# Optimization experiments

Measured on AMD Instinct MI355X. Metric: run time of the kernel, lower is better.

## Reference

```python
import jax, jax.numpy as jnp
import numpy as np

B, S, D, H = 8, 1024, 768, 12
DH = D // H
EPS = 1e-5


def setup_inputs() -> dict:
    key = jax.random.key(0)
    ks = jax.random.split(key, 12)
    sc_h = 1.0 / np.sqrt(DH)
    sc_d = 1.0 / np.sqrt(D)
    return {
        "x": jax.random.normal(ks[0], (B, S, D), jnp.float32),
        "ln1_g": jnp.ones((D,), jnp.float32),
        "ln1_b": jnp.zeros((D,), jnp.float32),
        "Wq": jax.random.normal(ks[1], (H, DH, DH), jnp.float32) * sc_h,
        "bq": jax.random.normal(ks[2], (H, DH), jnp.float32) * 0.01,
        "Wk": jax.random.normal(ks[3], (H, DH, DH), jnp.float32) * sc_h,
        "bk": jax.random.normal(ks[4], (H, DH), jnp.float32) * 0.01,
        "Wv": jax.random.normal(ks[5], (H, DH, DH), jnp.float32) * sc_h,
        "bv": jax.random.normal(ks[6], (H, DH), jnp.float32) * 0.01,
        "ln2_g": jnp.ones((D,), jnp.float32),
        "ln2_b": jnp.zeros((D,), jnp.float32),
        "W1": jax.random.normal(ks[7], (D, 4 * D), jnp.float32) * sc_d,  # c_fc (bias=False)
        "W2": jax.random.normal(ks[8], (4 * D, D), jnp.float32) * (1.0 / np.sqrt(4 * D)),  # c_proj (bias=False)
    }


def _layernorm(x, g, b):
    m = jnp.mean(x, axis=-1, keepdims=True)
    v = jnp.mean(jnp.square(x - m), axis=-1, keepdims=True)
    return (x - m) * jax.lax.rsqrt(v + EPS) * g + b


def _msa(x, Wq, bq, Wk, bk, Wv, bv):
    b, s, d = x.shape
    h = x.reshape(b, s, H, DH)  # per-head slices of the embedding
    q = jnp.einsum('bshd,hde->bhse', h, Wq) + bq[None, :, None, :]
    k = jnp.einsum('bshd,hde->bhse', h, Wk) + bk[None, :, None, :]
    v = jnp.einsum('bshd,hde->bhse', h, Wv) + bv[None, :, None, :]
    scores = jnp.einsum('bhse,bhte->bhst', q, k) / np.sqrt(DH).astype(np.float32)
    attn = jax.nn.softmax(scores, axis=-1)
    o = jnp.einsum('bhst,bhte->bhse', attn, v)
    return o.transpose(0, 2, 1, 3).reshape(b, s, d)  # concat heads


def reference(x, ln1_g, ln1_b, Wq, bq, Wk, bk, Wv, bv, ln2_g, ln2_b, W1, W2):
    out = x + _msa(_layernorm(x, ln1_g, ln1_b), Wq, bq, Wk, bk, Wv, bv)
    h = _layernorm(out, ln2_g, ln2_b)
    ffn = jnp.dot(jax.nn.gelu(jnp.dot(h, W1), approximate=False), W2)
    return out + ffn
```

## Files before the change

kernel.cpp:

```cpp
#include <hip/hip_runtime.h>
#include <hip/hip_bf16.h>
#include <math.h>

#define B_ 8
#define S_ 1024
#define D_ 768
#define H_ 12
#define QSCALE 0.18033688011112042f

typedef __attribute__((ext_vector_type(8))) short short8;
typedef __attribute__((ext_vector_type(4))) float floatx4;
typedef unsigned short ushort_t;

__device__ __forceinline__ ushort_t f2bf(float f) {
  unsigned int u = __builtin_bit_cast(unsigned int, f);
  u += 0x7fffu + ((u >> 16) & 1u);
  return (ushort_t)(u >> 16);
}

__device__ __forceinline__ unsigned int pkbf(float a, float b) {
  __hip_bfloat162 h = __float22bfloat162_rn(make_float2(a, b));
  unsigned int r;
  __builtin_memcpy(&r, &h, sizeof(r));
  return r;
}

__device__ __forceinline__ float gelu_f(float x) {
  const float z = fabsf(x) * 0.70710678118654752f;
  const float t = __builtin_amdgcn_rcpf(1.0f + 0.3275911f * z);
  const float p =
      t * (0.254829592f +
           t * (-0.284496736f +
                t * (1.421413741f + t * (-1.453152027f + t * 1.061405429f))));
  const float e = __expf(-z * z);
  const float erfv = 1.0f - p * e;
  return 0.5f * x * (1.0f + copysignf(erfv, x));
}

template <int N>
__device__ __forceinline__ void wait_vmcnt() {
  if constexpr (N == 0)
    asm volatile("s_waitcnt vmcnt(0)" ::: "memory");
  else if constexpr (N == 3)
    asm volatile("s_waitcnt vmcnt(3)" ::: "memory");
  else if constexpr (N == 4)
    asm volatile("s_waitcnt vmcnt(4)" ::: "memory");
  else if constexpr (N == 6)
    asm volatile("s_waitcnt vmcnt(6)" ::: "memory");
  else
    asm volatile("s_waitcnt vmcnt(8)" ::: "memory");
}

__global__ __launch_bounds__(256) void ln_bf16(
    const float* __restrict__ in, const float* __restrict__ g,
    const float* __restrict__ bias, ushort_t* __restrict__ out) {
  const int row = blockIdx.x * 4 + (threadIdx.x >> 6);
  const int lane = threadIdx.x & 63;
  const float* p = in + (size_t)row * D_;
  float4 v[3];
#pragma unroll
  for (int j = 0; j < 3; ++j) v[j] = *(const float4*)(p + j * 256 + lane * 4);
  float s = 0.f;
#pragma unroll
  for (int j = 0; j < 3; ++j) s += (v[j].x + v[j].y) + (v[j].z + v[j].w);
#pragma unroll
  for (int m = 1; m < 64; m <<= 1) s += __shfl_xor(s, m);
  const float mean = s * (1.0f / D_);
  float q = 0.f;
#pragma unroll
  for (int j = 0; j < 3; ++j) {
    const float a = v[j].x - mean, b = v[j].y - mean;
    const float c = v[j].z - mean, d = v[j].w - mean;
    q += (a * a + b * b) + (c * c + d * d);
  }
#pragma unroll
  for (int m = 1; m < 64; m <<= 1) q += __shfl_xor(q, m);
  const float rstd = rsqrtf(q * (1.0f / D_) + 1e-5f);
  ushort_t* o = out + (size_t)row * D_;
#pragma unroll
  for (int j = 0; j < 3; ++j) {
    const float4 gv = *(const float4*)(g + j * 256 + lane * 4);
    const float4 bv = *(const float4*)(bias + j * 256 + lane * 4);
    const unsigned int p01 = pkbf((v[j].x - mean) * rstd * gv.x + bv.x,
                                  (v[j].y - mean) * rstd * gv.y + bv.y);
    const unsigned int p23 = pkbf((v[j].z - mean) * rstd * gv.z + bv.z,
                                  (v[j].w - mean) * rstd * gv.w + bv.w);
    *(uint2*)(o + j * 256 + lane * 4) = make_uint2(p01, p23);
  }
}

__device__ __forceinline__ void tcast_body(
    const float* __restrict__ W, ushort_t* __restrict__ Wt,
    int Kdim, int Ndim, int bx, int by, float* sh) {
  float(*tile)[33] = (float(*)[33])sh;
  const int n0 = bx * 32, k0 = by * 32;
  const int tx = threadIdx.x & 31, ty = threadIdx.x >> 5;
#pragma unroll
  for (int i = 0; i < 32; i += 8)
    tile[ty + i][tx] = W[(size_t)(k0 + ty + i) * Ndim + n0 + tx];
  __syncthreads();
#pragma unroll
  for (int i = 0; i < 32; i += 8)
    Wt[(size_t)(n0 + ty + i) * Kdim + k0 + tx] = f2bf(tile[tx][ty + i]);
}

__global__ __launch_bounds__(256) void prep_weights(
    const float* __restrict__ W1, ushort_t* __restrict__ Wt1,
    const float* __restrict__ W2, ushort_t* __restrict__ Wt2,
    const float* __restrict__ Wq, const float* __restrict__ Wk,
    const float* __restrict__ Wv, ushort_t* __restrict__ Wqt,
    ushort_t* __restrict__ Wkt, ushort_t* __restrict__ Wvt) {
  __shared__ float sh[64 * 65];
  const int bid = blockIdx.x;
  if (bid < 2304) {
    tcast_body(W1, Wt1, 768, 3072, bid % 96, bid / 96, sh);
  } else if (bid < 4608) {
    const int idx = bid - 2304;
    tcast_body(W2, Wt2, 3072, 768, idx % 24, idx / 24, sh);
  } else {
    const int idx = bid - 4608;
    const int h = idx % 12, which = idx / 12;
    const float* W = which == 0 ? Wq : which == 1 ? Wk : Wv;
    ushort_t* O = which == 0 ? Wqt : which == 1 ? Wkt : Wvt;
    float(*t)[65] = (float(*)[65])sh;
    const int tid = threadIdx.x;
#pragma unroll
    for (int i = 0; i < 16; ++i) {
      const int idx2 = tid + i * 256;
      t[idx2 >> 6][idx2 & 63] = W[h * 4096 + idx2];
    }
    __syncthreads();
#pragma unroll
    for (int i = 0; i < 16; ++i) {
      const int idx2 = tid + i * 256;
      O[h * 4096 + idx2] = f2bf(t[idx2 & 63][idx2 >> 6]);
    }
  }
}

__global__ __launch_bounds__(256) void qkv_mfma(
    const ushort_t* __restrict__ xbf,
    const ushort_t* __restrict__ Wqt, const ushort_t* __restrict__ Wkt,
    const ushort_t* __restrict__ Wvt,
    const float* __restrict__ bq, const float* __restrict__ bk,
    const float* __restrict__ bv,
    ushort_t* __restrict__ qo, ushort_t* __restrict__ ko,
    ushort_t* __restrict__ vt) {
  const int h = blockIdx.y;
  const int mb = blockIdx.x * 128;
  const int tid = threadIdx.x;
  const int wave = tid >> 6, lane = tid & 63;
  const int lc = lane & 15, kq = lane >> 4;
  const int wm = wave * 32;

  __shared__ __align__(16) ushort_t Lb[4][2560];
  ushort_t* Lw = Lb[wave];

  short8 af[2][2];
#pragma unroll
  for (int mi = 0; mi < 2; ++mi)
#pragma unroll
    for (int kc = 0; kc < 2; ++kc)
      af[mi][kc] = *(const short8*)(xbf + (size_t)(mb + wm + mi * 16 + lc) * D_ +
                                    h * 64 + kc * 32 + kq * 8);

  const ushort_t* Wp[3] = {Wqt + h * 4096, Wkt + h * 4096, Wvt + h * 4096};
  floatx4 accT[2][2][4] = {};
  floatx4 accV[2][4] = {};
#pragma unroll
  for (int n = 0; n < 4; ++n)
#pragma unroll
    for (int kc = 0; kc < 2; ++kc) {
      const short8 wq_ = *(const short8*)(Wp[0] + (n * 16 + lc) * 64 +
                                          kc * 32 + kq * 8);
      const short8 wk_ = *(const short8*)(Wp[1] + (n * 16 + lc) * 64 +
                                          kc * 32 + kq * 8);
      const short8 wv_ = *(const short8*)(Wp[2] + (n * 16 + lc) * 64 +
                                          kc * 32 + kq * 8);
#pragma unroll
      for (int mi = 0; mi < 2; ++mi) {
        accT[0][mi][n] = __builtin_amdgcn_mfma_f32_16x16x32_bf16(
            wq_, af[mi][kc], accT[0][mi][n], 0, 0, 0);
        accT[1][mi][n] = __builtin_amdgcn_mfma_f32_16x16x32_bf16(
            wk_, af[mi][kc], accT[1][mi][n], 0, 0, 0);
        accV[mi][n] = __builtin_amdgcn_mfma_f32_16x16x32_bf16(
            af[mi][kc], wv_, accV[mi][n], 0, 0, 0);
      }
    }

  const int b = mb >> 10;
  const size_t obase = (size_t)(b * H_ + h) * (S_ * 64);
  const int sbase = (mb & 1023) + wm;

#pragma unroll
  for (int w3 = 0; w3 < 2; ++w3) {
    const float* bias = (w3 == 0 ? bq : bk) + h * 64;
    ushort_t* outp = w3 == 0 ? qo : ko;
#pragma unroll
    for (int mi = 0; mi < 2; ++mi)
#pragma unroll
      for (int n = 0; n < 4; ++n) {
        const float4 bv4 = *(const float4*)(bias + n * 16 + kq * 4);
        const floatx4 v = accT[w3][mi][n];
        float v0 = v[0] + bv4.x, v1 = v[1] + bv4.y;
        float v2 = v[2] + bv4.z, v3 = v[3] + bv4.w;
        if (w3 == 0) { v0 *= QSCALE; v1 *= QSCALE; v2 *= QSCALE; v3 *= QSCALE; }
        *(uint2*)(&Lw[(mi * 16 + lc) * 72 + n * 16 + kq * 4]) =
            make_uint2(pkbf(v0, v1), pkbf(v2, v3));
      }
    asm volatile("s_waitcnt lgkmcnt(0)" ::: "memory");
    const int srow = lane >> 2, c16 = (lane & 3) * 16;
#pragma unroll
    for (int it = 0; it < 2; ++it) {
      const int s = it * 16 + srow;
      const uint4 r0 = *(const uint4*)(&Lw[s * 72 + c16]);
      const uint4 r1 = *(const uint4*)(&Lw[s * 72 + c16 + 8]);
      *(uint4*)(outp + obase + (size_t)(sbase + s) * 64 + c16) = r0;
      *(uint4*)(outp + obase + (size_t)(sbase + s) * 64 + c16 + 8) = r1;
    }
    asm volatile("s_waitcnt lgkmcnt(0)" ::: "memory");
  }

#pragma unroll
  for (int n = 0; n < 4; ++n) {
    const float bvv = bv[h * 64 + n * 16 + lc];
#pragma unroll
    for (int mi = 0; mi < 2; ++mi) {
      const floatx4 v = accV[mi][n];
      *(uint2*)(&Lw[(n * 16 + lc) * 40 + mi * 16 + kq * 4]) =
          make_uint2(pkbf(v[0] + bvv, v[1] + bvv),
                     pkbf(v[2] + bvv, v[3] + bvv));
    }
  }
  asm volatile("s_waitcnt lgkmcnt(0)" ::: "memory");
  {
    const int erow = lane >> 2, s8 = (lane & 3) * 8;
#pragma unroll
    for (int it = 0; it < 4; ++it) {
      const int e = it * 16 + erow;
      const uint4 r0 = *(const uint4*)(&Lw[e * 40 + s8]);
      *(uint4*)(vt + obase + (size_t)e * S_ + sbase + s8) = r0;
    }
  }
}

__global__ __launch_bounds__(512) void attn_mfma(
    const ushort_t* __restrict__ qb, const ushort_t* __restrict__ kb,
    const ushort_t* __restrict__ vt, const float* __restrict__ x,
    float* __restrict__ out1) {
  const int bh = blockIdx.x;
  const int tid = threadIdx.x;
  const int wave = tid >> 6, lane = tid & 63;
  const int lc = lane & 15, kq = lane >> 4;
  const int q0 = blockIdx.y * 128 + wave * 16;

  __shared__ __align__(16) ushort_t smem[8192 + 8 * 16 * 72];
  ushort_t* Ks = smem;
  ushort_t* Vs = smem + 4096;
  ushort_t* Pp = smem + 8192 + wave * (16 * 72);

  const ushort_t* qp = qb + (size_t)bh * (S_ * 64);
  const ushort_t* kp = kb + (size_t)bh * (S_ * 64);
  const ushort_t* vp = vt + (size_t)bh * (S_ * 64);

  short8 qf[2];
#pragma unroll
  for (int kc = 0; kc < 2; ++kc)
    qf[kc] = *(const short8*)(qp + (size_t)(q0 + lc) * 64 + kc * 32 + kq * 8);

  const int srow = tid >> 3;
  const int sgc = ((tid & 7) ^ (srow & 7)) * 8;
  const int slds = srow * 64 + (tid & 7) * 8;
  const int swz = lc & 7;

  float l_r = 0.0f;
  floatx4 oacc[4] = {};

  for (int kt = 0; kt < 16; ++kt) {
    __builtin_amdgcn_global_load_lds(
        (const __attribute__((address_space(1))) unsigned int*)
            (kp + (size_t)(kt * 64 + srow) * 64 + sgc),
        (__attribute__((address_space(3))) unsigned int*)(Ks + slds), 16, 0, 0);
    __builtin_amdgcn_global_load_lds(
        (const __attribute__((address_space(1))) unsigned int*)
            (vp + (size_t)srow * S_ + kt * 64 + sgc),
        (__attribute__((address_space(3))) unsigned int*)(Vs + slds), 16, 0, 0);
    __syncthreads();

    floatx4 sacc[4] = {};
#pragma unroll
    for (int mi = 0; mi < 4; ++mi) {
      const int row = (mi * 16 + lc) * 64;
#pragma unroll
      for (int kc = 0; kc < 2; ++kc) {
        const short8 kf =
            *(const short8*)(Ks + row + ((kc * 4 + kq) ^ swz) * 8);
        sacc[mi] = __builtin_amdgcn_mfma_f32_16x16x32_bf16(
            kf, qf[kc], sacc[mi], 0, 0, 0);
      }
    }

    float pr[4][4];
    float sm = 0.f;
#pragma unroll
    for (int mi = 0; mi < 4; ++mi)
#pragma unroll
      for (int r = 0; r < 4; ++r) {
        pr[mi][r] = exp2f(sacc[mi][r]);
        sm += pr[mi][r];
      }
    l_r += sm;
#pragma unroll
    for (int mi = 0; mi < 4; ++mi) {
      const unsigned int p01 = pkbf(pr[mi][0], pr[mi][1]);
      const unsigned int p23 = pkbf(pr[mi][2], pr[mi][3]);
      *(uint2*)(&Pp[lc * 72 + mi * 16 + kq * 4]) = make_uint2(p01, p23);
    }
    asm volatile("s_waitcnt lgkmcnt(0)" ::: "memory");

    short8 pf[2];
#pragma unroll
    for (int kc = 0; kc < 2; ++kc)
      pf[kc] = *(const short8*)(&Pp[lc * 72 + kc * 32 + kq * 8]);
#pragma unroll
    for (int mi = 0; mi < 4; ++mi) {
      const int row = (mi * 16 + lc) * 64;
#pragma unroll
      for (int kc = 0; kc < 2; ++kc) {
        const short8 vf =
            *(const short8*)(Vs + row + ((kc * 4 + kq) ^ swz) * 8);
        oacc[mi] = __builtin_amdgcn_mfma_f32_16x16x32_bf16(
            vf, pf[kc], oacc[mi], 0, 0, 0);
      }
    }
    __syncthreads();
  }

  const int b = bh / H_, h = bh % H_;
  float lt = l_r;
  lt += __shfl_xor(lt, 16);
  lt += __shfl_xor(lt, 32);
  const float inv = 1.0f / lt;
  float* Ow = (float*)smem + wave * 1088;
#pragma unroll
  for (int mi = 0; mi < 4; ++mi) {
    floatx4 ov = oacc[mi];
    ov[0] *= inv; ov[1] *= inv; ov[2] *= inv; ov[3] *= inv;
    *(floatx4*)(&Ow[lc * 68 + mi * 16 + kq * 4]) = ov;
  }
  asm volatile("s_waitcnt lgkmcnt(0)" ::: "memory");
  const int row = (lane >> 3) & 7, c8 = (lane & 7) * 4;
#pragma unroll
  for (int rg = 0; rg < 2; ++rg) {
    const int qq = rg * 8 + row;
    const size_t gbase =
        ((size_t)(b * S_) + q0 + qq) * D_ + h * 64 + c8;
#pragma unroll
    for (int j = 0; j < 2; ++j) {
      const float4 ov = *(const float4*)(&Ow[qq * 68 + j * 32 + c8]);
      const float4 xv = *(const float4*)(x + gbase + j * 32);
      *(float4*)(out1 + gbase + j * 32) =
          make_float4(ov.x + xv.x, ov.y + xv.y, ov.z + xv.z, ov.w + xv.w);
    }
  }
}

template <int BM, int BN, int N, int K, bool GELU, bool RESID, bool OUT_BF16>
__global__ __launch_bounds__(512, 2) void gemm_tbuf(
    const ushort_t* __restrict__ A, const ushort_t* __restrict__ Bt,
    const float* __restrict__ resid, void* __restrict__ Cout) {
  constexpr int LPTA = BM / 64;
  constexpr int LPTB = BN / 64;
  constexpr int LPT = LPTA + LPTB;
  constexpr int NT = K / 64;
  constexpr int TSZ = (BM + BN) * 64;

  const int nb = blockIdx.x * BN;
  const int mb = blockIdx.y * BM;
  const int tid = threadIdx.x;
  const int wave = tid >> 6, lane = tid & 63;
  const int wm = (wave >> 1) * 64;
  const int wn = (wave & 1) * 64;

  __shared__ __align__(16) ushort_t Ls[3][TSZ];

  const int sr = tid >> 3;
  const int sc8 = (tid & 7) * 8;
  const int sgx = ((tid & 7) ^ (sr & 7)) * 8;

  auto stageAll = [&](int t, int buf) {
    const int kb = t * 64;
#pragma unroll
    for (int j = 0; j < LPTA; ++j) {
      const int row = j * 64 + sr;
      __builtin_amdgcn_global_load_lds(
          (const __attribute__((address_space(1))) unsigned int*)
              (A + (size_t)(mb + row) * K + kb + sgx),
          (__attribute__((address_space(3))) unsigned int*)
              (&Ls[buf][row * 64 + sc8]), 16, 0, 0);
    }
#pragma unroll
    for (int j = 0; j < LPTB; ++j) {
      const int row = j * 64 + sr;
      __builtin_amdgcn_global_load_lds(
          (const __attribute__((address_space(1))) unsigned int*)
              (Bt + (size_t)(nb + row) * K + kb + sgx),
          (__attribute__((address_space(3))) unsigned int*)
              (&Ls[buf][BM * 64 + row * 64 + sc8]), 16, 0, 0);
    }
  };

  stageAll(0, 0);
  stageAll(1, 1);
  wait_vmcnt<LPT>();
  __builtin_amdgcn_s_barrier();
  __builtin_amdgcn_sched_barrier(0);

  const int lc = lane & 15, kq = lane >> 4, swz = lc & 7;
  floatx4 acc[4][4] = {};

  int buf = 0;
#pragma unroll 1
  for (int t = 0; t < NT; ++t) {
    const ushort_t* As = &Ls[buf][0];
    const ushort_t* Bs = &Ls[buf][BM * 64];
    int nbuf = buf + 2; if (nbuf >= 3) nbuf -= 3;

    short8 af[4][2], bfr[4][2];
#pragma unroll
    for (int ks = 0; ks < 2; ++ks) {
#pragma unroll
      for (int i = 0; i < 4; ++i)
        af[i][ks] = *(const short8*)(As + (wm + i * 16 + lc) * 64 +
                                     ((ks * 4 + kq) ^ swz) * 8);
#pragma unroll
      for (int j = 0; j < 4; ++j)
        bfr[j][ks] = *(const short8*)(Bs + (wn + j * 16 + lc) * 64 +
                                      ((ks * 4 + kq) ^ swz) * 8);
    }
    if (t + 2 < NT) stageAll(t + 2, nbuf);
    __builtin_amdgcn_s_setprio(1);
#pragma unroll
    for (int ks = 0; ks < 2; ++ks)
#pragma unroll
      for (int i = 0; i < 4; ++i)
#pragma unroll
        for (int j = 0; j < 4; ++j)
          acc[i][j] = __builtin_amdgcn_mfma_f32_16x16x32_bf16(
              af[i][ks], bfr[j][ks], acc[i][j], 0, 0, 0);
    __builtin_amdgcn_s_setprio(0);
    if (t + 1 < NT) {
      if (t + 2 < NT)
        wait_vmcnt<LPT>();
      else
        wait_vmcnt<0>();
      __builtin_amdgcn_s_barrier();
      __builtin_amdgcn_sched_barrier(0);
    }
    buf = (buf == 2) ? 0 : buf + 1;
  }

  const int lcol = lane & 15, lr4 = (lane >> 4) * 4;
#pragma unroll
  for (int i = 0; i < 4; ++i)
#pragma unroll
    for (int r = 0; r < 4; ++r) {
      const int m = mb + wm + i * 16 + lr4 + r;
#pragma unroll
      for (int j = 0; j < 4; ++j) {
        const int col = nb + wn + j * 16 + lcol;
        float vv = acc[i][j][r];
        if (GELU) vv = gelu_f(vv);
        if (RESID) vv += resid[(size_t)m * N + col];
        if (OUT_BF16)
          ((ushort_t*)Cout)[(size_t)m * N + col] = f2bf(vv);
        else
          ((float*)Cout)[(size_t)m * N + col] = vv;
      }
    }
}

template <int BM, int BN, int N, int K, bool GELU, bool RESID, bool OUT_BF16,
          bool XCDMAP>
__global__ __launch_bounds__(512, 4) void gemm_pipe(
    const ushort_t* __restrict__ A, const ushort_t* __restrict__ Bt,
    const float* __restrict__ resid, void* __restrict__ Cout) {
  constexpr int MI = BM / 32;
  constexpr int NJ = BN / 64;
  constexpr int LPT = BM / 64 + BN / 64;
  constexpr int NT = K / 64;

  int mb, nb;
  if constexpr (XCDMAP) {
    const int lin = blockIdx.x;
    const int xcd = lin & 7, slot = lin >> 3;
    const int mbg = slot / (N / 128), nbi = slot - mbg * (N / 128);
    mb = (xcd * 16 + mbg) * 64;
    nb = nbi * 128;
  } else {
    nb = blockIdx.x * BN;
    mb = blockIdx.y * BM;
  }

  const int tid = threadIdx.x;
  const int wave = tid >> 6, lane = tid & 63;
  const int wm = (wave >> 2) * (BM / 2), wn = (wave & 3) * (BN / 4);

  __shared__ __align__(16) ushort_t Asp[2][BM * 64];
  __shared__ __align__(16) ushort_t Bsp[2][BN * 64];

  const int sr = tid >> 3;
  const int sc8 = (tid & 7) * 8;
  const int sgx = ((tid & 7) ^ (sr & 7)) * 8;

  auto stage = [&](int t, int buf) {
    const int kb = t * 64;
#pragma unroll
    for (int j = 0; j < BM / 64; ++j) {
      const int row = j * 64 + sr;
      __builtin_amdgcn_global_load_lds(
          (const __attribute__((address_space(1))) unsigned int*)
              (A + (size_t)(mb + row) * K + kb + sgx),
          (__attribute__((address_space(3))) unsigned int*)
              (&Asp[buf][row * 64 + sc8]), 16, 0, 0);
    }
#pragma unroll
    for (int j = 0; j < BN / 64; ++j) {
      const int row = j * 64 + sr;
      __builtin_amdgcn_global_load_lds(
          (const __attribute__((address_space(1))) unsigned int*)
              (Bt + (size_t)(nb + row) * K + kb + sgx),
          (__attribute__((address_space(3))) unsigned int*)
              (&Bsp[buf][row * 64 + sc8]), 16, 0, 0);
    }
  };

  stage(0, 0);
  stage(1, 1);
  wait_vmcnt<LPT>();
  __builtin_amdgcn_s_barrier();
  __builtin_amdgcn_sched_barrier(0);

  const int lc = lane & 15, kq = lane >> 4, swz = lc & 7;
  floatx4 acc[MI][NJ] = {};

#pragma unroll 1
  for (int t = 0; t < NT; ++t) {
    const int cur = t & 1;
    short8 af[MI][2], bfr[NJ][2];
#pragma unroll
    for (int ks = 0; ks < 2; ++ks) {
#pragma unroll
      for (int i = 0; i < MI; ++i)
        af[i][ks] = *(const short8*)(&Asp[cur][(wm + i * 16 + lc) * 64 +
                                               ((ks * 4 + kq) ^ swz) * 8]);
#pragma unroll
      for (int j = 0; j < NJ; ++j)
        bfr[j][ks] = *(const short8*)(&Bsp[cur][(wn + j * 16 + lc) * 64 +
                                                ((ks * 4 + kq) ^ swz) * 8]);
    }
    __builtin_amdgcn_s_setprio(1);
#pragma unroll
    for (int i = 0; i < MI; ++i)
#pragma unroll
      for (int j = 0; j < NJ; ++j)
        acc[i][j] = __builtin_amdgcn_mfma_f32_16x16x32_bf16(
            af[i][0], bfr[j][0], acc[i][j], 0, 0, 0);
    __builtin_amdgcn_s_setprio(0);
    asm volatile("s_waitcnt lgkmcnt(0)" ::: "memory");
    __builtin_amdgcn_sched_barrier(0);
    __builtin_amdgcn_s_barrier();
    __builtin_amdgcn_sched_barrier(0);
    if (t + 2 < NT) stage(t + 2, cur);
    __builtin_amdgcn_sched_barrier(0);
    if (t + 2 < NT)
      wait_vmcnt<LPT>();
    else if (t + 1 < NT)
      wait_vmcnt<0>();
    if (t + 1 < NT) {
      __builtin_amdgcn_s_barrier();
      __builtin_amdgcn_sched_barrier(0);
    }
    __builtin_amdgcn_s_setprio(1);
#pragma unroll
    for (int i = 0; i < MI; ++i)
#pragma unroll
      for (int j = 0; j < NJ; ++j)
        acc[i][j] = __builtin_amdgcn_mfma_f32_16x16x32_bf16(
            af[i][1], bfr[j][1], acc[i][j], 0, 0, 0);
    __builtin_amdgcn_s_setprio(0);
  }

  const int lcol = lane & 15, lr4 = (lane >> 4) * 4;
#pragma unroll
  for (int i = 0; i < MI; ++i)
#pragma unroll
    for (int r = 0; r < 4; ++r) {
      const int m = mb + wm + i * 16 + lr4 + r;
#pragma unroll
      for (int j = 0; j < NJ; ++j) {
        const int col = nb + wn + j * 16 + lcol;
        float vv = acc[i][j][r];
        if (GELU) vv = gelu_f(vv);
        if (RESID) vv += resid[(size_t)m * N + col];
        if (OUT_BF16)
          ((ushort_t*)Cout)[(size_t)m * N + col] = f2bf(vv);
        else
          ((float*)Cout)[(size_t)m * N + col] = vv;
      }
    }
}

extern "C" void kernel_launch(void* const* d_in, const int* in_sizes, int n_in,
                              void* d_out, int out_size, void* d_ws, size_t ws_size,
                              hipStream_t stream) {
  (void)in_sizes; (void)n_in; (void)out_size; (void)ws_size;
  const float* x     = (const float*)d_in[0];
  const float* ln1_g = (const float*)d_in[1];
  const float* ln1_b = (const float*)d_in[2];
  const float* Wq    = (const float*)d_in[3];
  const float* bq    = (const float*)d_in[4];
  const float* Wk    = (const float*)d_in[5];
  const float* bk    = (const float*)d_in[6];
  const float* Wv    = (const float*)d_in[7];
  const float* bv    = (const float*)d_in[8];
  const float* ln2_g = (const float*)d_in[9];
  const float* ln2_b = (const float*)d_in[10];
  const float* W1    = (const float*)d_in[11];
  const float* W2    = (const float*)d_in[12];
  float* out = (float*)d_out;

  const size_t n = (size_t)B_ * S_ * D_;
  ushort_t* u = (ushort_t*)d_ws;
  ushort_t* xbf  = u;
  ushort_t* qb   = xbf + n;
  ushort_t* kb   = qb + n;
  ushort_t* vt   = kb + n;
  ushort_t* xbf2 = vt + n;
  ushort_t* act  = xbf2 + n;
  ushort_t* Wt1  = act + (size_t)8192 * 3072;
  ushort_t* Wt2  = Wt1 + (size_t)3072 * 768;
  ushort_t* Wqt  = Wt2 + (size_t)768 * 3072;
  ushort_t* Wkt  = Wqt + H_ * 4096;
  ushort_t* Wvt  = Wkt + H_ * 4096;
  float* out1 = (float*)(Wvt + H_ * 4096);

  prep_weights<<<dim3(4644), dim3(256), 0, stream>>>(
      W1, Wt1, W2, Wt2, Wq, Wk, Wv, Wqt, Wkt, Wvt);
  ln_bf16<<<dim3(2048), dim3(256), 0, stream>>>(x, ln1_g, ln1_b, xbf);
  qkv_mfma<<<dim3(64, 12), dim3(256), 0, stream>>>(xbf, Wqt, Wkt, Wvt,
                                                   bq, bk, bv, qb, kb, vt);
  attn_mfma<<<dim3(96, 8), dim3(512), 0, stream>>>(qb, kb, vt, x, out1);
  ln_bf16<<<dim3(2048), dim3(256), 0, stream>>>(out1, ln2_g, ln2_b, xbf2);
  gemm_tbuf<256, 128, 3072, 768, true, false, true>
      <<<dim3(24, 32), dim3(512), 0, stream>>>(xbf2, Wt1, nullptr, act);
  gemm_pipe<64, 128, 768, 3072, false, true, false, true>
      <<<dim3(768), dim3(512), 0, stream>>>(act, Wt2, out1, out);
}
```

Before: 298.8 us.

## Split FFN1 GEMM K-step into four phased LDS-read/MFMA stages with staggered prefetch

Replaces the triple-buffered FFN1 GEMM with a variant using a 128x256 tile (waves arranged 2x4) and splits each K-step into four quadrant phases. Each phase loads part of the fragments from LDS, issues part of the next tile's global-to-LDS prefetch (A, then B halves), and runs a quarter of the MFMAs, with barriers between phases. The intent is to interleave LDS reads, global loads and matrix math more finely so they overlap better. It adds several extra workgroup barriers and lgkmcnt waits per K-step, which could stall waves.

```diff
diff --git a/kernel.cpp b/kernel.cpp
--- a/kernel.cpp
+++ b/kernel.cpp
@@ -365,13 +365,11 @@
   }
 }
 
-template <int BM, int BN, int N, int K, bool GELU, bool RESID, bool OUT_BF16>
-__global__ __launch_bounds__(512, 2) void gemm_tbuf(
+template <int N, int K, bool GELU, bool OUT_BF16>
+__global__ __launch_bounds__(512, 2) void gemm_8ph(
     const ushort_t* __restrict__ A, const ushort_t* __restrict__ Bt,
-    const float* __restrict__ resid, void* __restrict__ Cout) {
-  constexpr int LPTA = BM / 64;
-  constexpr int LPTB = BN / 64;
-  constexpr int LPT = LPTA + LPTB;
+    void* __restrict__ Cout) {
+  constexpr int BM = 128, BN = 256;
   constexpr int NT = K / 64;
   constexpr int TSZ = (BM + BN) * 64;
 
@@ -379,8 +377,8 @@
   const int mb = blockIdx.y * BM;
   const int tid = threadIdx.x;
   const int wave = tid >> 6, lane = tid & 63;
-  const int wm = (wave >> 1) * 64;
-  const int wn = (wave & 1) * 64;
+  const int wm = (wave >> 2) * 64;
+  const int wn = (wave & 3) * 64;
 
   __shared__ __align__(16) ushort_t Ls[3][TSZ];
 
@@ -388,10 +386,10 @@
   const int sc8 = (tid & 7) * 8;
   const int sgx = ((tid & 7) ^ (sr & 7)) * 8;
 
-  auto stageAll = [&](int t, int buf) {
+  auto stageA = [&](int t, int buf) {
     const int kb = t * 64;
 #pragma unroll
-    for (int j = 0; j < LPTA; ++j) {
+    for (int j = 0; j < 2; ++j) {
       const int row = j * 64 + sr;
       __builtin_amdgcn_global_load_lds(
           (const __attribute__((address_space(1))) unsigned int*)
@@ -399,9 +397,12 @@
           (__attribute__((address_space(3))) unsigned int*)
               (&Ls[buf][row * 64 + sc8]), 16, 0, 0);
     }
-#pragma unroll
-    for (int j = 0; j < LPTB; ++j) {
-      const int row = j * 64 + sr;
+  };
+  auto stageB = [&](int t, int buf, int half) {
+    const int kb = t * 64;
+#pragma unroll
+    for (int j = 0; j < 2; ++j) {
+      const int row = half * 128 + j * 64 + sr;
       __builtin_amdgcn_global_load_lds(
           (const __attribute__((address_space(1))) unsigned int*)
               (Bt + (size_t)(nb + row) * K + kb + sgx),
@@ -410,54 +411,118 @@
     }
   };
 
-  stageAll(0, 0);
-  stageAll(1, 1);
-  wait_vmcnt<LPT>();
+  stageA(0, 0); stageB(0, 0, 0); stageB(0, 0, 1);
+  stageA(1, 1); stageB(1, 1, 0); stageB(1, 1, 1);
+  wait_vmcnt<6>();
   __builtin_amdgcn_s_barrier();
   __builtin_amdgcn_sched_barrier(0);
 
   const int lc = lane & 15, kq = lane >> 4, swz = lc & 7;
   floatx4 acc[4][4] = {};
 
-  int buf = 0;
 #pragma unroll 1
   for (int t = 0; t < NT; ++t) {
+    const int buf = t % 3;
+    const int nbuf = (t + 2) % 3;
+    const bool pre = (t + 2 < NT);
     const ushort_t* As = &Ls[buf][0];
     const ushort_t* Bs = &Ls[buf][BM * 64];
-    int nbuf = buf + 2; if (nbuf >= 3) nbuf -= 3;
-
     short8 af[4][2], bfr[4][2];
-#pragma unroll
-    for (int ks = 0; ks < 2; ++ks) {
-#pragma unroll
-      for (int i = 0; i < 4; ++i)
+
+#pragma unroll
+    for (int i = 0; i < 2; ++i)
+#pragma unroll
+      for (int ks = 0; ks < 2; ++ks) {
         af[i][ks] = *(const short8*)(As + (wm + i * 16 + lc) * 64 +
                                      ((ks * 4 + kq) ^ swz) * 8);
-#pragma unroll
-      for (int j = 0; j < 4; ++j)
+        bfr[i][ks] = *(const short8*)(Bs + (wn + i * 16 + lc) * 64 +
+                                      ((ks * 4 + kq) ^ swz) * 8);
+      }
+    if (pre) stageA(t + 2, nbuf);
+    asm volatile("s_waitcnt lgkmcnt(0)" ::: "memory");
+    __builtin_amdgcn_sched_barrier(0);
+    __builtin_amdgcn_s_setprio(1);
+#pragma unroll
+    for (int i = 0; i < 2; ++i)
+#pragma unroll
+      for (int j = 0; j < 2; ++j) {
+        acc[i][j] = __builtin_amdgcn_mfma_f32_16x16x32_bf16(
+            af[i][0], bfr[j][0], acc[i][j], 0, 0, 0);
+        acc[i][j] = __builtin_amdgcn_mfma_f32_16x16x32_bf16(
+            af[i][1], bfr[j][1], acc[i][j], 0, 0, 0);
+      }
+    __builtin_amdgcn_s_setprio(0);
+    __builtin_amdgcn_sched_barrier(0);
+    __builtin_amdgcn_s_barrier();
+    __builtin_amdgcn_sched_barrier(0);
+
+#pragma unroll
+    for (int j = 2; j < 4; ++j)
+#pragma unroll
+      for (int ks = 0; ks < 2; ++ks)
         bfr[j][ks] = *(const short8*)(Bs + (wn + j * 16 + lc) * 64 +
                                       ((ks * 4 + kq) ^ swz) * 8);
-    }
-    if (t + 2 < NT) stageAll(t + 2, nbuf);
+    if (pre) stageB(t + 2, nbuf, 0);
+    asm volatile("s_waitcnt lgkmcnt(0)" ::: "memory");
+    __builtin_amdgcn_sched_barrier(0);
     __builtin_amdgcn_s_setprio(1);
 #pragma unroll
-    for (int ks = 0; ks < 2; ++ks)
-#pragma unroll
-      for (int i = 0; i < 4; ++i)
-#pragma unroll
-        for (int j = 0; j < 4; ++j)
-          acc[i][j] = __builtin_amdgcn_mfma_f32_16x16x32_bf16(
-              af[i][ks], bfr[j][ks], acc[i][j], 0, 0, 0);
+    for (int i = 0; i < 2; ++i)
+#pragma unroll
+      for (int j = 2; j < 4; ++j) {
+        acc[i][j] = __builtin_amdgcn_mfma_f32_16x16x32_bf16(
+            af[i][0], bfr[j][0], acc[i][j], 0, 0, 0);
+        acc[i][j] = __builtin_amdgcn_mfma_f32_16x16x32_bf16(
+            af[i][1], bfr[j][1], acc[i][j], 0, 0, 0);
+      }
+    __builtin_amdgcn_s_setprio(0);
+    __builtin_amdgcn_sched_barrier(0);
+    __builtin_amdgcn_s_barrier();
+    __builtin_amdgcn_sched_barrier(0);
+
+#pragma unroll
+    for (int i = 2; i < 4; ++i)
+#pragma unroll
+      for (int ks = 0; ks < 2; ++ks)
+        af[i][ks] = *(const short8*)(As + (wm + i * 16 + lc) * 64 +
+                                     ((ks * 4 + kq) ^ swz) * 8);
+    if (pre) stageB(t + 2, nbuf, 1);
+    asm volatile("s_waitcnt lgkmcnt(0)" ::: "memory");
+    __builtin_amdgcn_sched_barrier(0);
+    __builtin_amdgcn_s_setprio(1);
+#pragma unroll
+    for (int i = 2; i < 4; ++i)
+#pragma unroll
+      for (int j = 0; j < 2; ++j) {
+        acc[i][j] = __builtin_amdgcn_mfma_f32_16x16x32_bf16(
+            af[i][0], bfr[j][0], acc[i][j], 0, 0, 0);
+        acc[i][j] = __builtin_amdgcn_mfma_f32_16x16x32_bf16(
+            af[i][1], bfr[j][1], acc[i][j], 0, 0, 0);
+      }
+    __builtin_amdgcn_s_setprio(0);
+    __builtin_amdgcn_sched_barrier(0);
+    __builtin_amdgcn_s_barrier();
+    __builtin_amdgcn_sched_barrier(0);
+
+    __builtin_amdgcn_s_setprio(1);
+#pragma unroll
+    for (int i = 2; i < 4; ++i)
+#pragma unroll
+      for (int j = 2; j < 4; ++j) {
+        acc[i][j] = __builtin_amdgcn_mfma_f32_16x16x32_bf16(
+            af[i][0], bfr[j][0], acc[i][j], 0, 0, 0);
+        acc[i][j] = __builtin_amdgcn_mfma_f32_16x16x32_bf16(
+            af[i][1], bfr[j][1], acc[i][j], 0, 0, 0);
+      }
     __builtin_amdgcn_s_setprio(0);
     if (t + 1 < NT) {
-      if (t + 2 < NT)
-        wait_vmcnt<LPT>();
+      if (pre)
+        wait_vmcnt<6>();
       else
         wait_vmcnt<0>();
       __builtin_amdgcn_s_barrier();
       __builtin_amdgcn_sched_barrier(0);
     }
-    buf = (buf == 2) ? 0 : buf + 1;
   }
 
   const int lcol = lane & 15, lr4 = (lane >> 4) * 4;
@@ -471,7 +536,6 @@
         const int col = nb + wn + j * 16 + lcol;
         float vv = acc[i][j][r];
         if (GELU) vv = gelu_f(vv);
-        if (RESID) vv += resid[(size_t)m * N + col];
         if (OUT_BF16)
           ((ushort_t*)Cout)[(size_t)m * N + col] = f2bf(vv);
         else
@@ -652,8 +716,8 @@
                                                    bq, bk, bv, qb, kb, vt);
   attn_mfma<<<dim3(96, 8), dim3(512), 0, stream>>>(qb, kb, vt, x, out1);
   ln_bf16<<<dim3(2048), dim3(256), 0, stream>>>(out1, ln2_g, ln2_b, xbf2);
-  gemm_tbuf<256, 128, 3072, 768, true, false, true>
-      <<<dim3(24, 32), dim3(512), 0, stream>>>(xbf2, Wt1, nullptr, act);
+  gemm_8ph<3072, 768, true, true>
+      <<<dim3(12, 64), dim3(512), 0, stream>>>(xbf2, Wt1, act);
   gemm_pipe<64, 128, 768, 3072, false, true, false, true>
       <<<dim3(768), dim3(512), 0, stream>>>(act, Wt2, out1, out);
 }
```

Result: faster. 282.5 us (-5.5%).
